# Kernel optimization log

Hardware: AMD Instinct MI355X
Metric: run time of the kernel (lower is better)

The kernel has to match this reference:

```python
import jax, jax.numpy as jnp
import numpy as np


def setup_inputs() -> dict:
    key = jax.random.key(0)
    ks = jax.random.split(key, 5)
    T, H, I, E = 8192, 2048, 1408, 16
    return {
        "x": jax.random.normal(ks[0], (T, H), dtype=jnp.float32),
        "gate_w": jax.random.normal(ks[1], (E, H), dtype=jnp.float32) * 0.02,
        "W1": jax.random.normal(ks[2], (E, I, H), dtype=jnp.float32) * 0.02,
        "Up": jax.random.normal(ks[3], (E, I, H), dtype=jnp.float32) * 0.02,
        "W2": jax.random.normal(ks[4], (E, H, I), dtype=jnp.float32) * 0.02,
        "topk": 2,
    }


def reference(x, gate_w, W1, Up, W2, topk):
    # x: [T, H]; gate_w: [E, H]; W1/Up: [E, I, H]; W2: [E, H, I]
    E = gate_w.shape[0]
    logits = x @ gate_w.T                                   # [T, E]
    topk_w, topk_ids = jax.lax.top_k(logits, topk)          # [T, K]
    topk_w = jax.nn.softmax(topk_w, axis=-1)                # softmax over selected experts
    # combine weight per (token, expert): sum of routing weights where expert selected
    cw = jnp.sum(jax.nn.one_hot(topk_ids, E, dtype=x.dtype) * topk_w[..., None], axis=1)  # [T, E]

    def body(acc, inputs):
        w1, up, w2, we = inputs                             # [I,H],[I,H],[H,I],[T]
        h = jax.nn.silu(x @ w1.T) * (x @ up.T)              # [T, I]
        return acc + we[:, None] * (h @ w2.T), None

    out, _ = jax.lax.scan(body, jnp.zeros_like(x), (W1, Up, W2, cw.T))
    return out
```

## Files before the change

### kernel.cpp

```cpp
#include <hip/hip_runtime.h>

static constexpr int kT = 8192;
static constexpr int kH = 2048;
static constexpr int kI = 1408;
static constexpr int kE = 16;

typedef __bf16 bf16x8 __attribute__((ext_vector_type(8)));
typedef float floatx4 __attribute__((ext_vector_type(4)));

__device__ __forceinline__ __bf16 f2bf(float f) { return (__bf16)f; }

__global__ void cvt_x_kernel(const float* __restrict__ x, __bf16* __restrict__ xb) {
    size_t i = ((size_t)blockIdx.x * 256 + threadIdx.x) * 8;
    float4 v0 = *(const float4*)(x + i);
    float4 v1 = *(const float4*)(x + i + 4);
    union { __bf16 b[8]; uint4 u; } o;
    o.b[0] = f2bf(v0.x); o.b[1] = f2bf(v0.y); o.b[2] = f2bf(v0.z); o.b[3] = f2bf(v0.w);
    o.b[4] = f2bf(v1.x); o.b[5] = f2bf(v1.y); o.b[6] = f2bf(v1.z); o.b[7] = f2bf(v1.w);
    *(uint4*)(xb + i) = o.u;
}

__global__ __launch_bounds__(256)
void gate_kernel(const float* __restrict__ x, const float* __restrict__ gw,
                 int* __restrict__ t_ids, float* __restrict__ t_w,
                 int* __restrict__ counts) {
    const int lane = threadIdx.x & 63;
    const int t = blockIdx.x * 4 + (threadIdx.x >> 6);
    float acc[kE];
#pragma unroll
    for (int e = 0; e < kE; ++e) acc[e] = 0.f;
    const float* xr = x + (size_t)t * kH;
    for (int h = lane; h < kH; h += 64) {
        const float xv = xr[h];
#pragma unroll
        for (int e = 0; e < kE; ++e) acc[e] += xv * gw[e * kH + h];
    }
#pragma unroll
    for (int e = 0; e < kE; ++e) {
        float v = acc[e];
        for (int off = 32; off > 0; off >>= 1) v += __shfl_xor(v, off, 64);
        acc[e] = v;
    }
    if (lane == 0) {
        int i0 = 0; float l0 = acc[0];
#pragma unroll
        for (int e = 1; e < kE; ++e) if (acc[e] > l0) { l0 = acc[e]; i0 = e; }
        int i1 = -1; float l1 = -3.4e38f;
#pragma unroll
        for (int e = 0; e < kE; ++e) if (e != i0 && acc[e] > l1) { l1 = acc[e]; i1 = e; }
        const float ex = __expf(l1 - l0);
        const float inv = 1.f / (1.f + ex);
        t_ids[2 * t] = i0; t_ids[2 * t + 1] = i1;
        t_w[2 * t] = inv;  t_w[2 * t + 1] = ex * inv;
        atomicAdd(counts + i0, 1);
        atomicAdd(counts + i1, 1);
    }
}

__global__ void scan_kernel(const int* __restrict__ counts, int* __restrict__ offs,
                            int* __restrict__ fill) {
    if (threadIdx.x == 0) {
        int s = 0;
        for (int e = 0; e < kE; ++e) { offs[e] = s; fill[e] = s; s += counts[e]; }
        offs[kE] = s;
    }
}

__global__ void scatter_kernel(const int* __restrict__ t_ids, const float* __restrict__ t_w,
                               int* __restrict__ fill, int* __restrict__ btok,
                               float* __restrict__ bw) {
    int t = blockIdx.x * 256 + threadIdx.x;
    if (t < kT) {
#pragma unroll
        for (int k = 0; k < 2; ++k) {
            int e = t_ids[2 * t + k];
            int pos = atomicAdd(fill + e, 1);
            btok[pos] = t;
            bw[pos] = t_w[2 * t + k];
        }
    }
}

__global__ __launch_bounds__(256, 2)
void gemm1_kernel(const __bf16* __restrict__ xb, const float* __restrict__ W1,
                  const float* __restrict__ Up, const int* __restrict__ btok,
                  const float* __restrict__ bw, const int* __restrict__ offs,
                  __bf16* __restrict__ hbuf) {
    const int e = blockIdx.z;
    const int seg0 = offs[e];
    const int ne = offs[e + 1] - seg0;
    const int m0 = blockIdx.y * 128;
    if (m0 >= ne) return;
    const int n0 = blockIdx.x * 64;

    __shared__ __align__(16) __bf16 sA[128 * 64];
    __shared__ __align__(16) __bf16 sB1[64 * 64];
    __shared__ __align__(16) __bf16 sB2[64 * 64];

    const int tid = threadIdx.x;

    const int ar = tid >> 3;
    const int ac = (tid & 7) * 8;
    const __bf16* aptr[4];
#pragma unroll
    for (int i = 0; i < 4; ++i) {
        int rr = m0 + ar + 32 * i;
        if (rr >= ne) rr = ne - 1;
        aptr[i] = xb + (size_t)btok[seg0 + rr] * kH + ac;
    }

    const int brr = tid >> 4;
    const int bcc = (tid & 15) * 4;
    const float* b1p = W1 + ((size_t)e * kI + n0 + brr) * kH + bcc;
    const float* b2p = Up + ((size_t)e * kI + n0 + brr) * kH + bcc;

    const int wid = tid >> 6, lane = tid & 63;
    const int wm = (wid >> 1) * 64, wn = (wid & 1) * 32;
    const int lr = lane & 15;
    const int lk = (lane >> 4) * 8;

    floatx4 acc1[4][2], acc2[4][2];
#pragma unroll
    for (int i = 0; i < 4; ++i)
#pragma unroll
        for (int j = 0; j < 2; ++j) { acc1[i][j] = (floatx4)0.f; acc2[i][j] = (floatx4)0.f; }

    for (int k0 = 0; k0 < kH; k0 += 64) {
        __syncthreads();
#pragma unroll
        for (int i = 0; i < 4; ++i) {
            uint4 v = *(const uint4*)(aptr[i] + k0);
            *(uint4*)(sA + (ar + 32 * i) * 64 + ac) = v;
        }
#pragma unroll
        for (int i = 0; i < 4; ++i) {
            float4 v1 = *(const float4*)(b1p + (size_t)(16 * i) * kH + k0);
            float4 v2 = *(const float4*)(b2p + (size_t)(16 * i) * kH + k0);
            union { __bf16 b[4]; uint2 u; } o1, o2;
            o1.b[0] = f2bf(v1.x); o1.b[1] = f2bf(v1.y); o1.b[2] = f2bf(v1.z); o1.b[3] = f2bf(v1.w);
            o2.b[0] = f2bf(v2.x); o2.b[1] = f2bf(v2.y); o2.b[2] = f2bf(v2.z); o2.b[3] = f2bf(v2.w);
            *(uint2*)(sB1 + (brr + 16 * i) * 64 + bcc) = o1.u;
            *(uint2*)(sB2 + (brr + 16 * i) * 64 + bcc) = o2.u;
        }
        __syncthreads();
#pragma unroll
        for (int ks = 0; ks < 2; ++ks) {
            const int kk = ks * 32 + lk;
            bf16x8 af[4], bf1[2], bf2[2];
#pragma unroll
            for (int i = 0; i < 4; ++i)
                af[i] = *(const bf16x8*)(sA + (wm + i * 16 + lr) * 64 + kk);
#pragma unroll
            for (int j = 0; j < 2; ++j) {
                bf1[j] = *(const bf16x8*)(sB1 + (wn + j * 16 + lr) * 64 + kk);
                bf2[j] = *(const bf16x8*)(sB2 + (wn + j * 16 + lr) * 64 + kk);
            }
#pragma unroll
            for (int i = 0; i < 4; ++i)
#pragma unroll
                for (int j = 0; j < 2; ++j) {
                    acc1[i][j] = __builtin_amdgcn_mfma_f32_16x16x32_bf16(af[i], bf1[j], acc1[i][j], 0, 0, 0);
                    acc2[i][j] = __builtin_amdgcn_mfma_f32_16x16x32_bf16(af[i], bf2[j], acc2[i][j], 0, 0, 0);
                }
        }
    }

    const int q4 = (lane >> 4) * 4;
#pragma unroll
    for (int i = 0; i < 4; ++i) {
#pragma unroll
        for (int r = 0; r < 4; ++r) {
            const int row = wm + i * 16 + q4 + r;
            if (m0 + row < ne) {
                const float wrt = bw[seg0 + m0 + row];
                __bf16* hp = hbuf + (size_t)(seg0 + m0 + row) * kI + n0 + wn + (lane & 15);
#pragma unroll
                for (int j = 0; j < 2; ++j) {
                    float a = acc1[i][j][r];
                    float b = acc2[i][j][r];
                    float s = a / (1.f + __expf(-a));
                    hp[j * 16] = f2bf(s * b * wrt);
                }
            }
        }
    }
}

__global__ __launch_bounds__(256, 2)
void gemm2_kernel(const __bf16* __restrict__ hbuf, const float* __restrict__ W2,
                  const int* __restrict__ btok, const int* __restrict__ offs,
                  float* __restrict__ out) {
    const int e = blockIdx.z;
    const int seg0 = offs[e];
    const int ne = offs[e + 1] - seg0;
    const int m0 = blockIdx.y * 128;
    if (m0 >= ne) return;
    const int n0 = blockIdx.x * 64;

    __shared__ __align__(16) __bf16 sA[128 * 64];
    __shared__ __align__(16) __bf16 sB[64 * 64];

    const int tid = threadIdx.x;
    const int ar = tid >> 3;
    const int ac = (tid & 7) * 8;
    const __bf16* aptr[4];
#pragma unroll
    for (int i = 0; i < 4; ++i) {
        int rr = m0 + ar + 32 * i;
        if (rr >= ne) rr = ne - 1;
        aptr[i] = hbuf + (size_t)(seg0 + rr) * kI + ac;
    }

    const int brr = tid >> 4;
    const int bcc = (tid & 15) * 4;
    const float* bp = W2 + ((size_t)e * kH + n0 + brr) * kI + bcc;

    const int wid = tid >> 6, lane = tid & 63;
    const int wm = (wid >> 1) * 64, wn = (wid & 1) * 32;
    const int lr = lane & 15;
    const int lk = (lane >> 4) * 8;

    floatx4 acc[4][2];
#pragma unroll
    for (int i = 0; i < 4; ++i)
#pragma unroll
        for (int j = 0; j < 2; ++j) acc[i][j] = (floatx4)0.f;

    for (int k0 = 0; k0 < kI; k0 += 64) {
        __syncthreads();
#pragma unroll
        for (int i = 0; i < 4; ++i) {
            uint4 v = *(const uint4*)(aptr[i] + k0);
            *(uint4*)(sA + (ar + 32 * i) * 64 + ac) = v;
        }
#pragma unroll
        for (int i = 0; i < 4; ++i) {
            float4 v1 = *(const float4*)(bp + (size_t)(16 * i) * kI + k0);
            union { __bf16 b[4]; uint2 u; } o1;
            o1.b[0] = f2bf(v1.x); o1.b[1] = f2bf(v1.y); o1.b[2] = f2bf(v1.z); o1.b[3] = f2bf(v1.w);
            *(uint2*)(sB + (brr + 16 * i) * 64 + bcc) = o1.u;
        }
        __syncthreads();
#pragma unroll
        for (int ks = 0; ks < 2; ++ks) {
            const int kk = ks * 32 + lk;
            bf16x8 af[4], bfr[2];
#pragma unroll
            for (int i = 0; i < 4; ++i)
                af[i] = *(const bf16x8*)(sA + (wm + i * 16 + lr) * 64 + kk);
#pragma unroll
            for (int j = 0; j < 2; ++j)
                bfr[j] = *(const bf16x8*)(sB + (wn + j * 16 + lr) * 64 + kk);
#pragma unroll
            for (int i = 0; i < 4; ++i)
#pragma unroll
                for (int j = 0; j < 2; ++j)
                    acc[i][j] = __builtin_amdgcn_mfma_f32_16x16x32_bf16(af[i], bfr[j], acc[i][j], 0, 0, 0);
        }
    }

    const int q4 = (lane >> 4) * 4;
#pragma unroll
    for (int i = 0; i < 4; ++i) {
#pragma unroll
        for (int r = 0; r < 4; ++r) {
            const int row = wm + i * 16 + q4 + r;
            if (m0 + row < ne) {
                const int tok = btok[seg0 + m0 + row];
                float* op = out + (size_t)tok * kH + n0 + wn + (lane & 15);
#pragma unroll
                for (int j = 0; j < 2; ++j)
                    atomicAdd(op + j * 16, acc[i][j][r]);
            }
        }
    }
}

extern "C" void kernel_launch(void* const* d_in, const int* in_sizes, int n_in,
                              void* d_out, int out_size, void* d_ws, size_t ws_size,
                              hipStream_t stream) {
    const float* x  = (const float*)d_in[0];
    const float* gw = (const float*)d_in[1];
    const float* W1 = (const float*)d_in[2];
    const float* Up = (const float*)d_in[3];
    const float* W2 = (const float*)d_in[4];
    float* out = (float*)d_out;

    char* ws = (char*)d_ws;
    size_t o = 0;
    __bf16* xb   = (__bf16*)(ws + o); o += (size_t)kT * kH * 2;
    __bf16* hbuf = (__bf16*)(ws + o); o += (size_t)(2 * kT) * kI * 2;
    int*   t_ids = (int*)(ws + o);    o += (size_t)(2 * kT) * 4;
    float* t_w   = (float*)(ws + o);  o += (size_t)(2 * kT) * 4;
    int*   btok  = (int*)(ws + o);    o += (size_t)(2 * kT) * 4;
    float* bw    = (float*)(ws + o);  o += (size_t)(2 * kT) * 4;
    int*   counts = (int*)(ws + o);   o += 64;
    int*   offs   = (int*)(ws + o);   o += 128;
    int*   fill   = (int*)(ws + o);   o += 64;

    hipMemsetAsync(out, 0, (size_t)kT * kH * sizeof(float), stream);
    hipMemsetAsync(counts, 0, kE * sizeof(int), stream);

    cvt_x_kernel<<<(kT * kH / 8) / 256, 256, 0, stream>>>(x, xb);
    gate_kernel<<<kT / 4, 256, 0, stream>>>(x, gw, t_ids, t_w, counts);
    scan_kernel<<<1, 64, 0, stream>>>(counts, offs, fill);
    scatter_kernel<<<(kT + 255) / 256, 256, 0, stream>>>(t_ids, t_w, fill, btok, bw);

    dim3 g1(kI / 64, 64, kE);
    gemm1_kernel<<<g1, 256, 0, stream>>>(xb, W1, Up, btok, bw, offs, hbuf);
    dim3 g2(kH / 64, 64, kE);
    gemm2_kernel<<<g2, 256, 0, stream>>>(hbuf, W2, btok, offs, out);
}
```

Measured before the change: 1.641 ms.

## Pre-convert expert weights to bf16 and stage tiles via direct global-to-LDS loads

Adds separate passes that convert W1, Up and W2 to bf16 in workspace, reusing the W1 buffer for W2. The new GEMM kernels load tiles with global_load_lds into a k-chunked LDS layout and drop the in-loop fp32-to-bf16 conversion. Work is split across waves differently: gemm1 gives each wave one matrix (gate or up) and combines the two through LDS in the epilogue, and gemm2 uses a wider 128-column tile. The intent is to cut conversion and register-staging work in the GEMM loops, at the cost of extra full-weight conversion traffic each call. The old kernels remain as a fallback when the workspace is too small.

```diff
diff --git a/kernel.cpp b/kernel.cpp
--- a/kernel.cpp
+++ b/kernel.cpp
@@ -10,304 +10,516 @@
 
 __device__ __forceinline__ __bf16 f2bf(float f) { return (__bf16)f; }
 
-__global__ void cvt_x_kernel(const float* __restrict__ x, __bf16* __restrict__ xb) {
-    size_t i = ((size_t)blockIdx.x * 256 + threadIdx.x) * 8;
-    float4 v0 = *(const float4*)(x + i);
-    float4 v1 = *(const float4*)(x + i + 4);
-    union { __bf16 b[8]; uint4 u; } o;
-    o.b[0] = f2bf(v0.x); o.b[1] = f2bf(v0.y); o.b[2] = f2bf(v0.z); o.b[3] = f2bf(v0.w);
-    o.b[4] = f2bf(v1.x); o.b[5] = f2bf(v1.y); o.b[6] = f2bf(v1.z); o.b[7] = f2bf(v1.w);
-    *(uint4*)(xb + i) = o.u;
+__device__ __forceinline__ void gld16(const void* g, void* l) {
+  __builtin_amdgcn_global_load_lds(
+      (const __attribute__((address_space(1))) void*)g,
+      (__attribute__((address_space(3))) void*)l, 16, 0, 0);
+}
+
+__global__ void cvt_kernel(const float* __restrict__ src, __bf16* __restrict__ dst, long n8) {
+  long i = (long)blockIdx.x * 256 + threadIdx.x;
+  if (i >= n8) return;
+  size_t b = (size_t)i * 8;
+  float4 v0 = *(const float4*)(src + b);
+  float4 v1 = *(const float4*)(src + b + 4);
+  union { __bf16 h[8]; uint4 u; } o;
+  o.h[0] = f2bf(v0.x); o.h[1] = f2bf(v0.y); o.h[2] = f2bf(v0.z); o.h[3] = f2bf(v0.w);
+  o.h[4] = f2bf(v1.x); o.h[5] = f2bf(v1.y); o.h[6] = f2bf(v1.z); o.h[7] = f2bf(v1.w);
+  *(uint4*)(dst + b) = o.u;
 }
 
 __global__ __launch_bounds__(256)
 void gate_kernel(const float* __restrict__ x, const float* __restrict__ gw,
                  int* __restrict__ t_ids, float* __restrict__ t_w,
                  int* __restrict__ counts) {
-    const int lane = threadIdx.x & 63;
-    const int t = blockIdx.x * 4 + (threadIdx.x >> 6);
-    float acc[kE];
-#pragma unroll
-    for (int e = 0; e < kE; ++e) acc[e] = 0.f;
-    const float* xr = x + (size_t)t * kH;
-    for (int h = lane; h < kH; h += 64) {
-        const float xv = xr[h];
-#pragma unroll
-        for (int e = 0; e < kE; ++e) acc[e] += xv * gw[e * kH + h];
-    }
-#pragma unroll
-    for (int e = 0; e < kE; ++e) {
-        float v = acc[e];
-        for (int off = 32; off > 0; off >>= 1) v += __shfl_xor(v, off, 64);
-        acc[e] = v;
-    }
-    if (lane == 0) {
-        int i0 = 0; float l0 = acc[0];
-#pragma unroll
-        for (int e = 1; e < kE; ++e) if (acc[e] > l0) { l0 = acc[e]; i0 = e; }
-        int i1 = -1; float l1 = -3.4e38f;
-#pragma unroll
-        for (int e = 0; e < kE; ++e) if (e != i0 && acc[e] > l1) { l1 = acc[e]; i1 = e; }
-        const float ex = __expf(l1 - l0);
-        const float inv = 1.f / (1.f + ex);
-        t_ids[2 * t] = i0; t_ids[2 * t + 1] = i1;
-        t_w[2 * t] = inv;  t_w[2 * t + 1] = ex * inv;
-        atomicAdd(counts + i0, 1);
-        atomicAdd(counts + i1, 1);
-    }
+  const int lane = threadIdx.x & 63;
+  const int t = blockIdx.x * 4 + (threadIdx.x >> 6);
+  float acc[kE];
+#pragma unroll
+  for (int e = 0; e < kE; ++e) acc[e] = 0.f;
+  const float* xr = x + (size_t)t * kH;
+  for (int h = lane; h < kH; h += 64) {
+    const float xv = xr[h];
+#pragma unroll
+    for (int e = 0; e < kE; ++e) acc[e] += xv * gw[e * kH + h];
+  }
+#pragma unroll
+  for (int e = 0; e < kE; ++e) {
+    float v = acc[e];
+    for (int off = 32; off > 0; off >>= 1) v += __shfl_xor(v, off, 64);
+    acc[e] = v;
+  }
+  if (lane == 0) {
+    int i0 = 0; float l0 = acc[0];
+#pragma unroll
+    for (int e = 1; e < kE; ++e) if (acc[e] > l0) { l0 = acc[e]; i0 = e; }
+    int i1 = -1; float l1 = -3.4e38f;
+#pragma unroll
+    for (int e = 0; e < kE; ++e) if (e != i0 && acc[e] > l1) { l1 = acc[e]; i1 = e; }
+    const float ex = __expf(l1 - l0);
+    const float inv = 1.f / (1.f + ex);
+    t_ids[2 * t] = i0; t_ids[2 * t + 1] = i1;
+    t_w[2 * t] = inv;  t_w[2 * t + 1] = ex * inv;
+    atomicAdd(counts + i0, 1);
+    atomicAdd(counts + i1, 1);
+  }
 }
 
 __global__ void scan_kernel(const int* __restrict__ counts, int* __restrict__ offs,
                             int* __restrict__ fill) {
-    if (threadIdx.x == 0) {
-        int s = 0;
-        for (int e = 0; e < kE; ++e) { offs[e] = s; fill[e] = s; s += counts[e]; }
-        offs[kE] = s;
-    }
+  if (threadIdx.x == 0) {
+    int s = 0;
+    for (int e = 0; e < kE; ++e) { offs[e] = s; fill[e] = s; s += counts[e]; }
+    offs[kE] = s;
+  }
 }
 
 __global__ void scatter_kernel(const int* __restrict__ t_ids, const float* __restrict__ t_w,
                                int* __restrict__ fill, int* __restrict__ btok,
                                float* __restrict__ bw) {
-    int t = blockIdx.x * 256 + threadIdx.x;
-    if (t < kT) {
-#pragma unroll
-        for (int k = 0; k < 2; ++k) {
-            int e = t_ids[2 * t + k];
-            int pos = atomicAdd(fill + e, 1);
-            btok[pos] = t;
-            bw[pos] = t_w[2 * t + k];
+  int t = blockIdx.x * 256 + threadIdx.x;
+  if (t < kT) {
+#pragma unroll
+    for (int k = 0; k < 2; ++k) {
+      int e = t_ids[2 * t + k];
+      int pos = atomicAdd(fill + e, 1);
+      btok[pos] = t;
+      bw[pos] = t_w[2 * t + k];
+    }
+  }
+}
+
+
+__global__ __launch_bounds__(256, 2)
+void gemm1_main(const __bf16* __restrict__ xb, const __bf16* __restrict__ w1b,
+                const __bf16* __restrict__ upb, const int* __restrict__ btok,
+                const float* __restrict__ bw, const int* __restrict__ offs,
+                __bf16* __restrict__ hbuf) {
+  const int e = blockIdx.z;
+  const int seg0 = offs[e];
+  const int ne = offs[e + 1] - seg0;
+  const int m0 = blockIdx.y * 128;
+  if (m0 >= ne) return;
+  const int n0 = blockIdx.x * 64;
+
+  __shared__ __align__(16) __bf16 smem[16384];
+  __bf16* sA  = smem;
+  __bf16* sB1 = smem + 8192;
+  __bf16* sB2 = smem + 12288;
+
+  const int tid = threadIdx.x;
+  const int wid = tid >> 6, lane = tid & 63;
+  const int mat = wid >> 1;
+  const int wm = (wid & 1) * 64;
+  const int lr = lane & 15;
+  const int lq = lane >> 4;
+
+  const __bf16* gsrc;
+  __bf16* lbase;
+  int cstride;
+  if (wid < 2) {
+    int r = m0 + wid * 64 + lane; if (r >= ne) r = ne - 1;
+    gsrc = xb + (size_t)btok[seg0 + r] * kH;
+    lbase = sA + wid * 512;
+    cstride = 1024;
+  } else if (wid == 2) {
+    gsrc = w1b + ((size_t)e * kI + n0 + lane) * kH;
+    lbase = sB1;
+    cstride = 512;
+  } else {
+    gsrc = upb + ((size_t)e * kI + n0 + lane) * kH;
+    lbase = sB2;
+    cstride = 512;
+  }
+
+  floatx4 acc[4][4];
+#pragma unroll
+  for (int i = 0; i < 4; ++i)
+#pragma unroll
+    for (int j = 0; j < 4; ++j) acc[i][j] = (floatx4)0.f;
+
+  const __bf16* bmat = mat ? sB2 : sB1;
+
+  for (int k0 = 0; k0 < kH; k0 += 64) {
+#pragma unroll
+    for (int c = 0; c < 8; ++c)
+      gld16(gsrc + k0 + c * 8, lbase + c * cstride);
+    __syncthreads();
+#pragma unroll
+    for (int ks = 0; ks < 2; ++ks) {
+      const int c4 = ks * 4 + lq;
+      const __bf16* aB = sA + c4 * 1024 + (wm + lr) * 8;
+      const __bf16* bB = bmat + c4 * 512 + lr * 8;
+      bf16x8 af[4], bfr[4];
+#pragma unroll
+      for (int i = 0; i < 4; ++i) af[i] = *(const bf16x8*)(aB + i * 128);
+#pragma unroll
+      for (int j = 0; j < 4; ++j) bfr[j] = *(const bf16x8*)(bB + j * 128);
+#pragma unroll
+      for (int i = 0; i < 4; ++i)
+#pragma unroll
+        for (int j = 0; j < 4; ++j)
+          acc[i][j] = __builtin_amdgcn_mfma_f32_16x16x32_bf16(af[i], bfr[j], acc[i][j], 0, 0, 0);
+    }
+    __syncthreads();
+  }
+
+  float* sX = (float*)smem;
+  const int q4 = lq * 4;
+  if (mat == 1) {
+#pragma unroll
+    for (int i = 0; i < 4; ++i)
+#pragma unroll
+      for (int j = 0; j < 4; ++j)
+#pragma unroll
+        for (int r = 0; r < 4; ++r)
+          sX[(wm + i * 16 + q4 + r) * 64 + j * 16 + lr] = acc[i][j][r];
+  }
+  __syncthreads();
+  if (mat == 0) {
+#pragma unroll
+    for (int i = 0; i < 4; ++i) {
+#pragma unroll
+      for (int r = 0; r < 4; ++r) {
+        const int row = wm + i * 16 + q4 + r;
+        if (m0 + row < ne) {
+          const float wrt = bw[seg0 + m0 + row];
+          __bf16* hp = hbuf + (size_t)(seg0 + m0 + row) * kI + n0;
+#pragma unroll
+          for (int j = 0; j < 4; ++j) {
+            float a = acc[i][j][r];
+            float u = sX[row * 64 + j * 16 + lr];
+            float s = a / (1.f + __expf(-a));
+            hp[j * 16 + lr] = f2bf(s * u * wrt);
+          }
         }
-    }
+      }
+    }
+  }
 }
 
 __global__ __launch_bounds__(256, 2)
-void gemm1_kernel(const __bf16* __restrict__ xb, const float* __restrict__ W1,
-                  const float* __restrict__ Up, const int* __restrict__ btok,
-                  const float* __restrict__ bw, const int* __restrict__ offs,
-                  __bf16* __restrict__ hbuf) {
-    const int e = blockIdx.z;
-    const int seg0 = offs[e];
-    const int ne = offs[e + 1] - seg0;
-    const int m0 = blockIdx.y * 128;
-    if (m0 >= ne) return;
-    const int n0 = blockIdx.x * 64;
-
-    __shared__ __align__(16) __bf16 sA[128 * 64];
-    __shared__ __align__(16) __bf16 sB1[64 * 64];
-    __shared__ __align__(16) __bf16 sB2[64 * 64];
-
-    const int tid = threadIdx.x;
-
-    const int ar = tid >> 3;
-    const int ac = (tid & 7) * 8;
-    const __bf16* aptr[4];
+void gemm2_main(const __bf16* __restrict__ hbuf, const __bf16* __restrict__ w2b,
+                const int* __restrict__ btok, const int* __restrict__ offs,
+                float* __restrict__ out) {
+  const int e = blockIdx.z;
+  const int seg0 = offs[e];
+  const int ne = offs[e + 1] - seg0;
+  const int m0 = blockIdx.y * 128;
+  if (m0 >= ne) return;
+  const int n0 = blockIdx.x * 128;
+
+  __shared__ __align__(16) __bf16 smem2[16384];
+  __bf16* sA = smem2;
+  __bf16* sB = smem2 + 8192;
+
+  const int tid = threadIdx.x;
+  const int wid = tid >> 6, lane = tid & 63;
+  const int wm = (wid & 1) * 64;
+  const int wn = (wid >> 1) * 64;
+  const int lr = lane & 15;
+  const int lq = lane >> 4;
+
+  const __bf16* gsrc;
+  __bf16* lbase;
+  if (wid < 2) {
+    int r = m0 + wid * 64 + lane; if (r >= ne) r = ne - 1;
+    gsrc = hbuf + (size_t)(seg0 + r) * kI;
+    lbase = sA + wid * 512;
+  } else {
+    gsrc = w2b + ((size_t)e * kH + n0 + (wid - 2) * 64 + lane) * kI;
+    lbase = sB + (wid - 2) * 512;
+  }
+
+  floatx4 acc[4][4];
+#pragma unroll
+  for (int i = 0; i < 4; ++i)
+#pragma unroll
+    for (int j = 0; j < 4; ++j) acc[i][j] = (floatx4)0.f;
+
+  for (int k0 = 0; k0 < kI; k0 += 64) {
+#pragma unroll
+    for (int c = 0; c < 8; ++c)
+      gld16(gsrc + k0 + c * 8, lbase + c * 1024);
+    __syncthreads();
+#pragma unroll
+    for (int ks = 0; ks < 2; ++ks) {
+      const int c4 = ks * 4 + lq;
+      const __bf16* aB = sA + c4 * 1024 + (wm + lr) * 8;
+      const __bf16* bB = sB + c4 * 1024 + (wn + lr) * 8;
+      bf16x8 af[4], bfr[4];
+#pragma unroll
+      for (int i = 0; i < 4; ++i) af[i] = *(const bf16x8*)(aB + i * 128);
+#pragma unroll
+      for (int j = 0; j < 4; ++j) bfr[j] = *(const bf16x8*)(bB + j * 128);
+#pragma unroll
+      for (int i = 0; i < 4; ++i)
+#pragma unroll
+        for (int j = 0; j < 4; ++j)
+          acc[i][j] = __builtin_amdgcn_mfma_f32_16x16x32_bf16(af[i], bfr[j], acc[i][j], 0, 0, 0);
+    }
+    __syncthreads();
+  }
+
+  const int q4 = lq * 4;
+#pragma unroll
+  for (int i = 0; i < 4; ++i) {
+#pragma unroll
+    for (int r = 0; r < 4; ++r) {
+      const int row = wm + i * 16 + q4 + r;
+      if (m0 + row < ne) {
+        const int tok = btok[seg0 + m0 + row];
+        float* op = out + (size_t)tok * kH + n0 + wn;
+#pragma unroll
+        for (int j = 0; j < 4; ++j)
+          atomicAdd(op + j * 16 + lr, acc[i][j][r]);
+      }
+    }
+  }
+}
+
+__global__ __launch_bounds__(256, 2)
+void gemm1_fb(const __bf16* __restrict__ xb, const float* __restrict__ W1,
+              const float* __restrict__ Up, const int* __restrict__ btok,
+              const float* __restrict__ bw, const int* __restrict__ offs,
+              __bf16* __restrict__ hbuf) {
+  const int e = blockIdx.z;
+  const int seg0 = offs[e];
+  const int ne = offs[e + 1] - seg0;
+  const int m0 = blockIdx.y * 128;
+  if (m0 >= ne) return;
+  const int n0 = blockIdx.x * 64;
+
+  __shared__ __align__(16) __bf16 sA[128 * 64];
+  __shared__ __align__(16) __bf16 sB1[64 * 64];
+  __shared__ __align__(16) __bf16 sB2[64 * 64];
+
+  const int tid = threadIdx.x;
+  const int ar = tid >> 3;
+  const int ac = (tid & 7) * 8;
+  const __bf16* aptr[4];
+#pragma unroll
+  for (int i = 0; i < 4; ++i) {
+    int rr = m0 + ar + 32 * i;
+    if (rr >= ne) rr = ne - 1;
+    aptr[i] = xb + (size_t)btok[seg0 + rr] * kH + ac;
+  }
+  const int brr = tid >> 4;
+  const int bcc = (tid & 15) * 4;
+  const float* b1p = W1 + ((size_t)e * kI + n0 + brr) * kH + bcc;
+  const float* b2p = Up + ((size_t)e * kI + n0 + brr) * kH + bcc;
+
+  const int wid = tid >> 6, lane = tid & 63;
+  const int wm = (wid >> 1) * 64, wn = (wid & 1) * 32;
+  const int lr = lane & 15;
+  const int lk = (lane >> 4) * 8;
+
+  floatx4 acc1[4][2], acc2[4][2];
+#pragma unroll
+  for (int i = 0; i < 4; ++i)
+#pragma unroll
+    for (int j = 0; j < 2; ++j) { acc1[i][j] = (floatx4)0.f; acc2[i][j] = (floatx4)0.f; }
+
+  for (int k0 = 0; k0 < kH; k0 += 64) {
+    __syncthreads();
 #pragma unroll
     for (int i = 0; i < 4; ++i) {
-        int rr = m0 + ar + 32 * i;
-        if (rr >= ne) rr = ne - 1;
-        aptr[i] = xb + (size_t)btok[seg0 + rr] * kH + ac;
-    }
-
-    const int brr = tid >> 4;
-    const int bcc = (tid & 15) * 4;
-    const float* b1p = W1 + ((size_t)e * kI + n0 + brr) * kH + bcc;
-    const float* b2p = Up + ((size_t)e * kI + n0 + brr) * kH + bcc;
-
-    const int wid = tid >> 6, lane = tid & 63;
-    const int wm = (wid >> 1) * 64, wn = (wid & 1) * 32;
-    const int lr = lane & 15;
-    const int lk = (lane >> 4) * 8;
-
-    floatx4 acc1[4][2], acc2[4][2];
-#pragma unroll
-    for (int i = 0; i < 4; ++i)
-#pragma unroll
-        for (int j = 0; j < 2; ++j) { acc1[i][j] = (floatx4)0.f; acc2[i][j] = (floatx4)0.f; }
-
-    for (int k0 = 0; k0 < kH; k0 += 64) {
-        __syncthreads();
-#pragma unroll
-        for (int i = 0; i < 4; ++i) {
-            uint4 v = *(const uint4*)(aptr[i] + k0);
-            *(uint4*)(sA + (ar + 32 * i) * 64 + ac) = v;
+      uint4 v = *(const uint4*)(aptr[i] + k0);
+      *(uint4*)(sA + (ar + 32 * i) * 64 + ac) = v;
+    }
+#pragma unroll
+    for (int i = 0; i < 4; ++i) {
+      float4 v1 = *(const float4*)(b1p + (size_t)(16 * i) * kH + k0);
+      float4 v2 = *(const float4*)(b2p + (size_t)(16 * i) * kH + k0);
+      union { __bf16 b[4]; uint2 u; } o1, o2;
+      o1.b[0] = f2bf(v1.x); o1.b[1] = f2bf(v1.y); o1.b[2] = f2bf(v1.z); o1.b[3] = f2bf(v1.w);
+      o2.b[0] = f2bf(v2.x); o2.b[1] = f2bf(v2.y); o2.b[2] = f2bf(v2.z); o2.b[3] = f2bf(v2.w);
+      *(uint2*)(sB1 + (brr + 16 * i) * 64 + bcc) = o1.u;
+      *(uint2*)(sB2 + (brr + 16 * i) * 64 + bcc) = o2.u;
+    }
+    __syncthreads();
+#pragma unroll
+    for (int ks = 0; ks < 2; ++ks) {
+      const int kk = ks * 32 + lk;
+      bf16x8 af[4], bf1[2], bf2[2];
+#pragma unroll
+      for (int i = 0; i < 4; ++i)
+        af[i] = *(const bf16x8*)(sA + (wm + i * 16 + lr) * 64 + kk);
+#pragma unroll
+      for (int j = 0; j < 2; ++j) {
+        bf1[j] = *(const bf16x8*)(sB1 + (wn + j * 16 + lr) * 64 + kk);
+        bf2[j] = *(const bf16x8*)(sB2 + (wn + j * 16 + lr) * 64 + kk);
+      }
+#pragma unroll
+      for (int i = 0; i < 4; ++i)
+#pragma unroll
+        for (int j = 0; j < 2; ++j) {
+          acc1[i][j] = __builtin_amdgcn_mfma_f32_16x16x32_bf16(af[i], bf1[j], acc1[i][j], 0, 0, 0);
+          acc2[i][j] = __builtin_amdgcn_mfma_f32_16x16x32_bf16(af[i], bf2[j], acc2[i][j], 0, 0, 0);
         }
-#pragma unroll
-        for (int i = 0; i < 4; ++i) {
-            float4 v1 = *(const float4*)(b1p + (size_t)(16 * i) * kH + k0);
-            float4 v2 = *(const float4*)(b2p + (size_t)(16 * i) * kH + k0);
-            union { __bf16 b[4]; uint2 u; } o1, o2;
-            o1.b[0] = f2bf(v1.x); o1.b[1] = f2bf(v1.y); o1.b[2] = f2bf(v1.z); o1.b[3] = f2bf(v1.w);
-            o2.b[0] = f2bf(v2.x); o2.b[1] = f2bf(v2.y); o2.b[2] = f2bf(v2.z); o2.b[3] = f2bf(v2.w);
-            *(uint2*)(sB1 + (brr + 16 * i) * 64 + bcc) = o1.u;
-            *(uint2*)(sB2 + (brr + 16 * i) * 64 + bcc) = o2.u;
+    }
+  }
+  const int q4 = (lane >> 4) * 4;
+#pragma unroll
+  for (int i = 0; i < 4; ++i) {
+#pragma unroll
+    for (int r = 0; r < 4; ++r) {
+      const int row = wm + i * 16 + q4 + r;
+      if (m0 + row < ne) {
+        const float wrt = bw[seg0 + m0 + row];
+        __bf16* hp = hbuf + (size_t)(seg0 + m0 + row) * kI + n0 + wn + (lane & 15);
+#pragma unroll
+        for (int j = 0; j < 2; ++j) {
+          float a = acc1[i][j][r];
+          float b = acc2[i][j][r];
+          float s = a / (1.f + __expf(-a));
+          hp[j * 16] = f2bf(s * b * wrt);
         }
-        __syncthreads();
-#pragma unroll
-        for (int ks = 0; ks < 2; ++ks) {
-            const int kk = ks * 32 + lk;
-            bf16x8 af[4], bf1[2], bf2[2];
-#pragma unroll
-            for (int i = 0; i < 4; ++i)
-                af[i] = *(const bf16x8*)(sA + (wm + i * 16 + lr) * 64 + kk);
-#pragma unroll
-            for (int j = 0; j < 2; ++j) {
-                bf1[j] = *(const bf16x8*)(sB1 + (wn + j * 16 + lr) * 64 + kk);
-                bf2[j] = *(const bf16x8*)(sB2 + (wn + j * 16 + lr) * 64 + kk);
-            }
-#pragma unroll
-            for (int i = 0; i < 4; ++i)
-#pragma unroll
-                for (int j = 0; j < 2; ++j) {
-                    acc1[i][j] = __builtin_amdgcn_mfma_f32_16x16x32_bf16(af[i], bf1[j], acc1[i][j], 0, 0, 0);
-                    acc2[i][j] = __builtin_amdgcn_mfma_f32_16x16x32_bf16(af[i], bf2[j], acc2[i][j], 0, 0, 0);
-                }
-        }
-    }
-
-    const int q4 = (lane >> 4) * 4;
+      }
+    }
+  }
+}
+
+__global__ __launch_bounds__(256, 2)
+void gemm2_fb(const __bf16* __restrict__ hbuf, const float* __restrict__ W2,
+              const int* __restrict__ btok, const int* __restrict__ offs,
+              float* __restrict__ out) {
+  const int e = blockIdx.z;
+  const int seg0 = offs[e];
+  const int ne = offs[e + 1] - seg0;
+  const int m0 = blockIdx.y * 128;
+  if (m0 >= ne) return;
+  const int n0 = blockIdx.x * 64;
+
+  __shared__ __align__(16) __bf16 sA[128 * 64];
+  __shared__ __align__(16) __bf16 sB[64 * 64];
+
+  const int tid = threadIdx.x;
+  const int ar = tid >> 3;
+  const int ac = (tid & 7) * 8;
+  const __bf16* aptr[4];
+#pragma unroll
+  for (int i = 0; i < 4; ++i) {
+    int rr = m0 + ar + 32 * i;
+    if (rr >= ne) rr = ne - 1;
+    aptr[i] = hbuf + (size_t)(seg0 + rr) * kI + ac;
+  }
+  const int brr = tid >> 4;
+  const int bcc = (tid & 15) * 4;
+  const float* bp = W2 + ((size_t)e * kH + n0 + brr) * kI + bcc;
+
+  const int wid = tid >> 6, lane = tid & 63;
+  const int wm = (wid >> 1) * 64, wn = (wid & 1) * 32;
+  const int lr = lane & 15;
+  const int lk = (lane >> 4) * 8;
+
+  floatx4 acc[4][2];
+#pragma unroll
+  for (int i = 0; i < 4; ++i)
+#pragma unroll
+    for (int j = 0; j < 2; ++j) acc[i][j] = (floatx4)0.f;
+
+  for (int k0 = 0; k0 < kI; k0 += 64) {
+    __syncthreads();
 #pragma unroll
     for (int i = 0; i < 4; ++i) {
-#pragma unroll
-        for (int r = 0; r < 4; ++r) {
-            const int row = wm + i * 16 + q4 + r;
-            if (m0 + row < ne) {
-                const float wrt = bw[seg0 + m0 + row];
-                __bf16* hp = hbuf + (size_t)(seg0 + m0 + row) * kI + n0 + wn + (lane & 15);
-#pragma unroll
-                for (int j = 0; j < 2; ++j) {
-                    float a = acc1[i][j][r];
-                    float b = acc2[i][j][r];
-                    float s = a / (1.f + __expf(-a));
-                    hp[j * 16] = f2bf(s * b * wrt);
-                }
-            }
-        }
-    }
-}
-
-__global__ __launch_bounds__(256, 2)
-void gemm2_kernel(const __bf16* __restrict__ hbuf, const float* __restrict__ W2,
-                  const int* __restrict__ btok, const int* __restrict__ offs,
-                  float* __restrict__ out) {
-    const int e = blockIdx.z;
-    const int seg0 = offs[e];
-    const int ne = offs[e + 1] - seg0;
-    const int m0 = blockIdx.y * 128;
-    if (m0 >= ne) return;
-    const int n0 = blockIdx.x * 64;
-
-    __shared__ __align__(16) __bf16 sA[128 * 64];
-    __shared__ __align__(16) __bf16 sB[64 * 64];
-
-    const int tid = threadIdx.x;
-    const int ar = tid >> 3;
-    const int ac = (tid & 7) * 8;
-    const __bf16* aptr[4];
+      uint4 v = *(const uint4*)(aptr[i] + k0);
+      *(uint4*)(sA + (ar + 32 * i) * 64 + ac) = v;
+    }
 #pragma unroll
     for (int i = 0; i < 4; ++i) {
-        int rr = m0 + ar + 32 * i;
-        if (rr >= ne) rr = ne - 1;
-        aptr[i] = hbuf + (size_t)(seg0 + rr) * kI + ac;
-    }
-
-    const int brr = tid >> 4;
-    const int bcc = (tid & 15) * 4;
-    const float* bp = W2 + ((size_t)e * kH + n0 + brr) * kI + bcc;
-
-    const int wid = tid >> 6, lane = tid & 63;
-    const int wm = (wid >> 1) * 64, wn = (wid & 1) * 32;
-    const int lr = lane & 15;
-    const int lk = (lane >> 4) * 8;
-
-    floatx4 acc[4][2];
-#pragma unroll
-    for (int i = 0; i < 4; ++i)
-#pragma unroll
-        for (int j = 0; j < 2; ++j) acc[i][j] = (floatx4)0.f;
-
-    for (int k0 = 0; k0 < kI; k0 += 64) {
-        __syncthreads();
-#pragma unroll
-        for (int i = 0; i < 4; ++i) {
-            uint4 v = *(const uint4*)(aptr[i] + k0);
-            *(uint4*)(sA + (ar + 32 * i) * 64 + ac) = v;
-        }
-#pragma unroll
-        for (int i = 0; i < 4; ++i) {
-            float4 v1 = *(const float4*)(bp + (size_t)(16 * i) * kI + k0);
-            union { __bf16 b[4]; uint2 u; } o1;
-            o1.b[0] = f2bf(v1.x); o1.b[1] = f2bf(v1.y); o1.b[2] = f2bf(v1.z); o1.b[3] = f2bf(v1.w);
-            *(uint2*)(sB + (brr + 16 * i) * 64 + bcc) = o1.u;
-        }
-        __syncthreads();
-#pragma unroll
-        for (int ks = 0; ks < 2; ++ks) {
-            const int kk = ks * 32 + lk;
-            bf16x8 af[4], bfr[2];
-#pragma unroll
-            for (int i = 0; i < 4; ++i)
-                af[i] = *(const bf16x8*)(sA + (wm + i * 16 + lr) * 64 + kk);
-#pragma unroll
-            for (int j = 0; j < 2; ++j)
-                bfr[j] = *(const bf16x8*)(sB + (wn + j * 16 + lr) * 64 + kk);
-#pragma unroll
-            for (int i = 0; i < 4; ++i)
-#pragma unroll
-                for (int j = 0; j < 2; ++j)
-                    acc[i][j] = __builtin_amdgcn_mfma_f32_16x16x32_bf16(af[i], bfr[j], acc[i][j], 0, 0, 0);
-        }
-    }
-
-    const int q4 = (lane >> 4) * 4;
-#pragma unroll
-    for (int i = 0; i < 4; ++i) {
-#pragma unroll
-        for (int r = 0; r < 4; ++r) {
-            const int row = wm + i * 16 + q4 + r;
-            if (m0 + row < ne) {
-                const int tok = btok[seg0 + m0 + row];
-                float* op = out + (size_t)tok * kH + n0 + wn + (lane & 15);
-#pragma unroll
-                for (int j = 0; j < 2; ++j)
-                    atomicAdd(op + j * 16, acc[i][j][r]);
-            }
-        }
-    }
+      float4 v1 = *(const float4*)(bp + (size_t)(16 * i) * kI + k0);
+      union { __bf16 b[4]; uint2 u; } o1;
+      o1.b[0] = f2bf(v1.x); o1.b[1] = f2bf(v1.y); o1.b[2] = f2bf(v1.z); o1.b[3] = f2bf(v1.w);
+      *(uint2*)(sB + (brr + 16 * i) * 64 + bcc) = o1.u;
+    }
+    __syncthreads();
+#pragma unroll
+    for (int ks = 0; ks < 2; ++ks) {
+      const int kk = ks * 32 + lk;
+      bf16x8 af[4], bfr[2];
+#pragma unroll
+      for (int i = 0; i < 4; ++i)
+        af[i] = *(const bf16x8*)(sA + (wm + i * 16 + lr) * 64 + kk);
+#pragma unroll
+      for (int j = 0; j < 2; ++j)
+        bfr[j] = *(const bf16x8*)(sB + (wn + j * 16 + lr) * 64 + kk);
+#pragma unroll
+      for (int i = 0; i < 4; ++i)
+#pragma unroll
+        for (int j = 0; j < 2; ++j)
+          acc[i][j] = __builtin_amdgcn_mfma_f32_16x16x32_bf16(af[i], bfr[j], acc[i][j], 0, 0, 0);
+    }
+  }
+  const int q4 = (lane >> 4) * 4;
+#pragma unroll
+  for (int i = 0; i < 4; ++i) {
+#pragma unroll
+    for (int r = 0; r < 4; ++r) {
+      const int row = wm + i * 16 + q4 + r;
+      if (m0 + row < ne) {
+        const int tok = btok[seg0 + m0 + row];
+        float* op = out + (size_t)tok * kH + n0 + wn + (lane & 15);
+#pragma unroll
+        for (int j = 0; j < 2; ++j)
+          atomicAdd(op + j * 16, acc[i][j][r]);
+      }
+    }
+  }
 }
 
 extern "C" void kernel_launch(void* const* d_in, const int* in_sizes, int n_in,
                               void* d_out, int out_size, void* d_ws, size_t ws_size,
                               hipStream_t stream) {
-    const float* x  = (const float*)d_in[0];
-    const float* gw = (const float*)d_in[1];
-    const float* W1 = (const float*)d_in[2];
-    const float* Up = (const float*)d_in[3];
-    const float* W2 = (const float*)d_in[4];
-    float* out = (float*)d_out;
-
-    char* ws = (char*)d_ws;
-    size_t o = 0;
-    __bf16* xb   = (__bf16*)(ws + o); o += (size_t)kT * kH * 2;
-    __bf16* hbuf = (__bf16*)(ws + o); o += (size_t)(2 * kT) * kI * 2;
-    int*   t_ids = (int*)(ws + o);    o += (size_t)(2 * kT) * 4;
-    float* t_w   = (float*)(ws + o);  o += (size_t)(2 * kT) * 4;
-    int*   btok  = (int*)(ws + o);    o += (size_t)(2 * kT) * 4;
-    float* bw    = (float*)(ws + o);  o += (size_t)(2 * kT) * 4;
-    int*   counts = (int*)(ws + o);   o += 64;
-    int*   offs   = (int*)(ws + o);   o += 128;
-    int*   fill   = (int*)(ws + o);   o += 64;
-
-    hipMemsetAsync(out, 0, (size_t)kT * kH * sizeof(float), stream);
-    hipMemsetAsync(counts, 0, kE * sizeof(int), stream);
-
-    cvt_x_kernel<<<(kT * kH / 8) / 256, 256, 0, stream>>>(x, xb);
-    gate_kernel<<<kT / 4, 256, 0, stream>>>(x, gw, t_ids, t_w, counts);
-    scan_kernel<<<1, 64, 0, stream>>>(counts, offs, fill);
-    scatter_kernel<<<(kT + 255) / 256, 256, 0, stream>>>(t_ids, t_w, fill, btok, bw);
-
+  const float* x  = (const float*)d_in[0];
+  const float* gw = (const float*)d_in[1];
+  const float* W1 = (const float*)d_in[2];
+  const float* Up = (const float*)d_in[3];
+  const float* W2 = (const float*)d_in[4];
+  float* out = (float*)d_out;
+
+  char* ws = (char*)d_ws;
+  size_t o = 0;
+  auto carve = [&](size_t bytes) -> char* {
+    char* p = ws + o; o += (bytes + 255) & ~(size_t)255; return p;
+  };
+
+  int*    t_ids = (int*)carve((size_t)2 * kT * 4);
+  float*  t_w   = (float*)carve((size_t)2 * kT * 4);
+  int*    btok  = (int*)carve((size_t)2 * kT * 4);
+  float*  bw    = (float*)carve((size_t)2 * kT * 4);
+  int*    counts= (int*)carve(kE * 4);
+  int*    offs  = (int*)carve((kE + 1) * 4);
+  int*    fill  = (int*)carve(kE * 4);
+  __bf16* xb    = (__bf16*)carve((size_t)kT * kH * 2);
+  __bf16* hbuf  = (__bf16*)carve((size_t)2 * kT * kI * 2);
+  __bf16* w1b   = (__bf16*)carve((size_t)kE * kI * kH * 2);
+  __bf16* upb   = (__bf16*)carve((size_t)kE * kI * kH * 2);
+  const size_t main_need = o;
+  __bf16* w2b = w1b;
+
+  hipMemsetAsync(out, 0, (size_t)kT * kH * 4, stream);
+  hipMemsetAsync(counts, 0, kE * 4, stream);
+
+  cvt_kernel<<<8192, 256, 0, stream>>>(x, xb, (long)kT * kH / 8);
+  gate_kernel<<<kT / 4, 256, 0, stream>>>(x, gw, t_ids, t_w, counts);
+  scan_kernel<<<1, 64, 0, stream>>>(counts, offs, fill);
+  scatter_kernel<<<(kT + 255) / 256, 256, 0, stream>>>(t_ids, t_w, fill, btok, bw);
+
+  if (ws_size >= main_need) {
+    const long w8 = (long)kE * kI * kH / 8;
+    const int wblocks = (int)((w8 + 255) / 256);
+    cvt_kernel<<<wblocks, 256, 0, stream>>>(W1, w1b, w8);
+    cvt_kernel<<<wblocks, 256, 0, stream>>>(Up, upb, w8);
     dim3 g1(kI / 64, 64, kE);
-    gemm1_kernel<<<g1, 256, 0, stream>>>(xb, W1, Up, btok, bw, offs, hbuf);
+    gemm1_main<<<g1, 256, 0, stream>>>(xb, w1b, upb, btok, bw, offs, hbuf);
+    cvt_kernel<<<wblocks, 256, 0, stream>>>(W2, w2b, w8);
+    dim3 g2(kH / 128, 64, kE);
+    gemm2_main<<<g2, 256, 0, stream>>>(hbuf, w2b, btok, offs, out);
+  } else {
+    dim3 g1(kI / 64, 64, kE);
+    gemm1_fb<<<g1, 256, 0, stream>>>(xb, W1, Up, btok, bw, offs, hbuf);
     dim3 g2(kH / 64, 64, kE);
-    gemm2_kernel<<<g2, 256, 0, stream>>>(hbuf, W2, btok, offs, out);
-}
+    gemm2_fb<<<g2, 256, 0, stream>>>(hbuf, W2, btok, offs, out);
+  }
+}
```

Result: slower. 1.738 ms (+5.9%).
